# Kernel tuning notes

Hardware: AMD Instinct MI355X
Metric: run time of the kernel (lower is better)

Reference implementation:

```python
import jax, jax.numpy as jnp
import numpy as np

E, K, MULT = 8, 2, 4          # num_experts, top_k, ffn mult
CF = 1.25                     # capacity_factor


def setup_inputs() -> dict:
    key = jax.random.key(0)
    ks = jax.random.split(key, 8)
    B, T, C = 4, 2048, 1024
    H = C * MULT
    s = 0.02
    return {
        "x": jax.random.normal(ks[0], (B, T, C), jnp.float32),
        "rw": jax.random.normal(ks[1], (E, C), jnp.float32) * s,   # router weight [E,C]
        "rb": jnp.zeros((E,), jnp.float32),                        # router bias
        "w1": jax.random.normal(ks[2], (E, C, H), jnp.float32) * s,
        "b1": jnp.zeros((E, H), jnp.float32),
        "w2": jax.random.normal(ks[3], (E, H, C), jnp.float32) * s,
        "b2": jnp.zeros((E, C), jnp.float32),
    }


def reference(x, rw, rb, w1, b1, w2, b2):
    B, T, C = x.shape
    N = B * T
    cap = int(CF * N / E)                      # static capacity per expert
    xf = x.reshape(N, C)
    logits = xf @ rw.T + rb                    # [N,E]
    probs = jax.nn.softmax(logits, axis=-1)
    topk_probs, topk_idx = jax.lax.top_k(probs, K)      # [N,K]
    topk_probs = topk_probs / topk_probs.sum(-1, keepdims=True)

    # Flatten (token, choice) row-major == torch.where(mask) ordering
    flat_idx = topk_idx.reshape(-1)            # [N*K] expert id per slot
    flat_gate = topk_probs.reshape(-1)         # [N*K]
    onehot = jax.nn.one_hot(flat_idx, E, dtype=jnp.int32)          # [N*K,E]
    pos = (jnp.cumsum(onehot, axis=0) - 1)[jnp.arange(N * K), flat_idx]  # rank within expert
    keep = pos < cap                           # first-come-first-served capacity drop
    tok = jnp.arange(N * K) // K               # owning token of each slot

    # Dispatch into [E, cap] buffers; dropped slots go to a dump slot at the end
    buf = jnp.where(keep, flat_idx * cap + pos, E * cap)
    gate_buf = jnp.zeros(E * cap + 1, x.dtype).at[buf].add(flat_gate)[:E * cap]
    tok_buf = jnp.zeros(E * cap + 1, jnp.int32).at[buf].set(tok)[:E * cap]

    inp = xf[tok_buf].reshape(E, cap, C)       # gathered expert inputs
    h = jax.nn.gelu(jnp.einsum('eic,ech->eih', inp, w1) + b1[:, None, :], approximate=False)
    out = jnp.einsum('eih,ehc->eic', h, w2) + b2[:, None, :]
    out = out * gate_buf.reshape(E, cap, 1)    # empty slots have gate 0 -> zero contribution

    y = jnp.zeros((N, C), x.dtype).at[tok_buf].add(out.reshape(E * cap, C))

    # Aux load-balancing loss
    imp = probs.sum(0)
    imp = imp / imp.sum()
    load = jnp.minimum(onehot.sum(0).astype(x.dtype), cap)   # kept token counts
    load = load / load.sum()
    aux_loss = (imp * load).sum() * (E ** 2)
    return y.reshape(B, T, C), aux_loss
```

## Files before the change

kernel.cpp:

```cpp
#include <hip/hip_runtime.h>
#include <hip/hip_bf16.h>
#include <math.h>

#define NE    8
#define KTOP  2
#define CDIM  1024
#define HDIM  4096
#define NTOK  8192
#define CAPE  1280
#define NSLOT (NTOK * KTOP)

typedef __bf16 bf16x8 __attribute__((ext_vector_type(8)));
typedef __bf16 bf16x4 __attribute__((ext_vector_type(4)));
typedef float  f32x4  __attribute__((ext_vector_type(4)));

__global__ __launch_bounds__(256) void k_transpose_bf16(
    const float* __restrict__ src, __bf16* __restrict__ dst, int R, int Cc)
{
    __shared__ float tile[32][33];
    const int e  = blockIdx.z;
    const int cb = blockIdx.x * 32;
    const int rb = blockIdx.y * 32;
    const int tx = threadIdx.x, ty = threadIdx.y;
    const float* s = src + (size_t)e * R * Cc;
    __bf16*      d = dst + (size_t)e * R * Cc;
#pragma unroll
    for (int i = 0; i < 32; i += 8)
        tile[ty + i][tx] = s[(size_t)(rb + ty + i) * Cc + cb + tx];
    __syncthreads();
#pragma unroll
    for (int i = 0; i < 32; i += 8)
        d[(size_t)(cb + ty + i) * R + rb + tx] = (__bf16)tile[tx][ty + i];
}

__global__ __launch_bounds__(256) void k_router(
    const float* __restrict__ x, const float* __restrict__ rw,
    const float* __restrict__ rb, float* __restrict__ probs,
    float* __restrict__ gates, int* __restrict__ tidx)
{
    __shared__ float rws[NE * CDIM];
    const int tid = threadIdx.x;
    for (int i = tid; i < NE * CDIM / 4; i += 256)
        ((float4*)rws)[i] = ((const float4*)rw)[i];
    __syncthreads();

    const int wave = tid >> 6, lane = tid & 63;
    const int n = blockIdx.x * 4 + wave;
    const float* xr = x + (size_t)n * CDIM;

    float acc[NE];
#pragma unroll
    for (int e = 0; e < NE; ++e) acc[e] = 0.f;
    for (int j = 0; j < CDIM / 64; ++j) {
        const float xv = xr[j * 64 + lane];
#pragma unroll
        for (int e = 0; e < NE; ++e) acc[e] += xv * rws[e * CDIM + j * 64 + lane];
    }
#pragma unroll
    for (int off = 32; off > 0; off >>= 1) {
#pragma unroll
        for (int e = 0; e < NE; ++e) acc[e] += __shfl_down(acc[e], off);
    }
    if (lane == 0) {
        float mx = -1e30f;
#pragma unroll
        for (int e = 0; e < NE; ++e) { acc[e] += rb[e]; mx = fmaxf(mx, acc[e]); }
        float p[NE], s = 0.f;
#pragma unroll
        for (int e = 0; e < NE; ++e) { p[e] = expf(acc[e] - mx); s += p[e]; }
        const float inv = 1.f / s;
#pragma unroll
        for (int e = 0; e < NE; ++e) { p[e] *= inv; probs[(size_t)n * NE + e] = p[e]; }
        int   i1 = 0;  float v1 = p[0];
        int   i2 = -1; float v2 = -1.f;
#pragma unroll
        for (int e = 1; e < NE; ++e) {
            if (p[e] > v1)      { v2 = v1; i2 = i1; v1 = p[e]; i1 = e; }
            else if (p[e] > v2) { v2 = p[e]; i2 = e; }
        }
        const float gs = 1.f / (v1 + v2);
        gates[n * 2 + 0] = v1 * gs;  gates[n * 2 + 1] = v2 * gs;
        tidx[n * 2 + 0]  = i1;       tidx[n * 2 + 1]  = i2;
    }
}

__global__ __launch_bounds__(256) void k_scan(
    const int* __restrict__ tidx, const float* __restrict__ probs,
    int* __restrict__ slot, int* __restrict__ tok, float* __restrict__ d_aux)
{
    __shared__ int   lcnt[256][NE];
    __shared__ float ps[256][NE];
    const int t = threadIdx.x;

    for (int i = t; i < NE * CAPE; i += 256) tok[i] = 0;

    int c8[NE];
#pragma unroll
    for (int e = 0; e < NE; ++e) c8[e] = 0;
    const int per  = NSLOT / 256;
    const int base = t * per;
    for (int s = 0; s < per; ++s) c8[tidx[base + s]]++;
#pragma unroll
    for (int e = 0; e < NE; ++e) lcnt[t][e] = c8[e];

    float f8[NE];
#pragma unroll
    for (int e = 0; e < NE; ++e) f8[e] = 0.f;
    for (int n = t; n < NTOK; n += 256) {
        const float4 a = *(const float4*)(probs + (size_t)n * NE);
        const float4 b = *(const float4*)(probs + (size_t)n * NE + 4);
        f8[0] += a.x; f8[1] += a.y; f8[2] += a.z; f8[3] += a.w;
        f8[4] += b.x; f8[5] += b.y; f8[6] += b.z; f8[7] += b.w;
    }
#pragma unroll
    for (int e = 0; e < NE; ++e) ps[t][e] = f8[e];

    __syncthreads();

    int pre[NE], tot[NE];
#pragma unroll
    for (int e = 0; e < NE; ++e) { pre[e] = 0; tot[e] = 0; }
    for (int tt = 0; tt < 256; ++tt) {
#pragma unroll
        for (int e = 0; e < NE; ++e) {
            const int v = lcnt[tt][e];
            tot[e] += v;
            if (tt < t) pre[e] += v;
        }
    }
    for (int s = 0; s < per; ++s) {
        const int sg = base + s;
        const int e  = tidx[sg];
        const int p  = pre[e]++;
        if (p < CAPE) { slot[sg] = e * CAPE + p; tok[e * CAPE + p] = sg >> 1; }
        else          { slot[sg] = -1; }
    }
    if (t == 0) {
        float imp[NE], isum = 0.f, ld[NE], lsum = 0.f;
#pragma unroll
        for (int e = 0; e < NE; ++e) {
            float v = 0.f;
            for (int tt = 0; tt < 256; ++tt) v += ps[tt][e];
            imp[e] = v; isum += v;
        }
#pragma unroll
        for (int e = 0; e < NE; ++e) { ld[e] = fminf((float)tot[e], (float)CAPE); lsum += ld[e]; }
        float aux = 0.f;
#pragma unroll
        for (int e = 0; e < NE; ++e) aux += (imp[e] / isum) * (ld[e] / lsum);
        *d_aux = aux * (float)(NE * NE);
    }
}

__global__ __launch_bounds__(256) void k_gather(
    const float* __restrict__ x, const int* __restrict__ tok,
    __bf16* __restrict__ inp)
{
    const int row = blockIdx.x;
    const int t   = threadIdx.x;
    const int tk  = tok[row];
    const float4 v = ((const float4*)(x + (size_t)tk * CDIM))[t];
    bf16x4 o;
    o[0] = (__bf16)v.x; o[1] = (__bf16)v.y; o[2] = (__bf16)v.z; o[3] = (__bf16)v.w;
    *(bf16x4*)(inp + (size_t)row * CDIM + t * 4) = o;
}

#define MFMA_BF16 __builtin_amdgcn_mfma_f32_16x16x32_bf16

template <bool GELU>
__global__ __launch_bounds__(512, 2) void k_gemm8(
    const __bf16* __restrict__ Aall, const __bf16* __restrict__ Ball,
    const float* __restrict__ biasAll, __bf16* __restrict__ Call,
    int Ktot, int Ntot, int NBN, int mtPerE)
{
    __shared__ char lds[131072];

    const int NK  = Ktot >> 6;
    const int nwg = gridDim.x;
    const int cpx = nwg >> 3;
    const int id  = blockIdx.x;
    const int sid = (id & 7) * cpx + (id >> 3);
    const int bm  = sid / NBN, bn = sid % NBN;
    const int e   = bm / mtPerE;

    const size_t row0 = (size_t)bm * 256;
    const int    col0 = bn * 256;

    const __bf16* gA = Aall + row0 * (size_t)Ktot;
    const __bf16* gB = Ball + ((size_t)e * Ntot + col0) * (size_t)Ktot;

    const int tid = threadIdx.x;
    const int w   = tid >> 6, l = tid & 63;
    const int wr  = w >> 2, wc = w & 3;
    const int lr  = l & 15, hi = l >> 4;

    const int srow = (w << 3) + (l >> 3);
    const int kf   = ((l & 7) ^ (l >> 3)) << 3;
    const int swz = (l & 7) << 4;
    const int kb0 = (hi << 4) ^ swz;
    const int kb1 = (64 + (hi << 4)) ^ swz;

    auto STAGE = [&](int buf, int op, int half, int kt) {
        const __bf16* g = (op ? gB : gA)
            + (size_t)(half * 128 + srow) * Ktot + kt * 64 + kf;
        char* d = lds + ((((buf << 1) + op) << 1) + half) * 16384 + w * 1024;
        __builtin_amdgcn_global_load_lds(
            (const __attribute__((address_space(1))) void*)g,
            (__attribute__((address_space(3))) void*)d, 16, 0, 0);
        __builtin_amdgcn_global_load_lds(
            (const __attribute__((address_space(1))) void*)(g + (size_t)64 * Ktot),
            (__attribute__((address_space(3))) void*)(d + 8192), 16, 0, 0);
    };

    STAGE(0, 0, 0, 0); STAGE(0, 0, 1, 0);
    STAGE(0, 1, 0, 0); STAGE(0, 1, 1, 0);
    if (NK > 1) {
        STAGE(1, 1, 0, 1); STAGE(1, 1, 1, 1);
        asm volatile("s_waitcnt vmcnt(4)" ::: "memory");
    } else {
        asm volatile("s_waitcnt vmcnt(0)" ::: "memory");
    }
    __builtin_amdgcn_s_barrier();
    __builtin_amdgcn_sched_barrier(0);

    f32x4 acc[8][4] = {};
    bf16x8 bfr[4][2], a[2][2];

#define PHASE_MFMA(MB)                                                        \
    __builtin_amdgcn_s_barrier();                                             \
    asm volatile("s_waitcnt lgkmcnt(0)" ::: "memory");                        \
    __builtin_amdgcn_sched_barrier(0);                                        \
    __builtin_amdgcn_s_setprio(1);                                            \
    _Pragma("unroll")                                                         \
    for (int mm = 0; mm < 2; ++mm) {                                          \
        _Pragma("unroll")                                                     \
        for (int n = 0; n < 4; ++n) {                                         \
            acc[(MB) + mm][n] = MFMA_BF16(bfr[n][0], a[mm][0], acc[(MB) + mm][n], 0, 0, 0); \
            acc[(MB) + mm][n] = MFMA_BF16(bfr[n][1], a[mm][1], acc[(MB) + mm][n], 0, 0, 0); \
        }                                                                     \
    }                                                                         \
    __builtin_amdgcn_s_setprio(0);                                            \
    __builtin_amdgcn_s_barrier();                                             \
    __builtin_amdgcn_sched_barrier(0);

#define LOAD_A(MB)                                                            \
    _Pragma("unroll")                                                         \
    for (int mm = 0; mm < 2; ++mm) {                                          \
        a[mm][0] = *(const bf16x8*)(Ab + ((MB) + mm) * 2048 + kb0);           \
        a[mm][1] = *(const bf16x8*)(Ab + ((MB) + mm) * 2048 + kb1);           \
    }

#pragma unroll 2
    for (int T = 0; T < NK; ++T) {
        const int cur = T & 1, nxt = cur ^ 1;
        const char* Ab = lds + (((cur << 1) + 0) * 2 + wr) * 16384 + lr * 128;
        const char* Bb = lds + (((cur << 1) + 1) * 2 + (wc >> 1)) * 16384
                             + (wc & 1) * 8192 + lr * 128;

#pragma unroll
        for (int n = 0; n < 4; ++n) {
            bfr[n][0] = *(const bf16x8*)(Bb + n * 2048 + kb0);
            bfr[n][1] = *(const bf16x8*)(Bb + n * 2048 + kb1);
        }
        LOAD_A(0)
        if (T + 1 < NK) STAGE(nxt, 0, 0, T + 1);
        PHASE_MFMA(0)

        LOAD_A(2)
        if (T + 1 < NK) STAGE(nxt, 0, 1, T + 1);
        PHASE_MFMA(2)

        LOAD_A(4)
        if (T + 2 < NK) STAGE(cur, 1, 0, T + 2);
        PHASE_MFMA(4)

        LOAD_A(6)
        if (T + 2 < NK) {
            STAGE(cur, 1, 1, T + 2);
            asm volatile("s_waitcnt vmcnt(4)" ::: "memory");
        } else if (T + 1 < NK) {
            asm volatile("s_waitcnt vmcnt(0)" ::: "memory");
        }
        PHASE_MFMA(6)
    }

    const size_t crow0 = row0 + (size_t)wr * 128;
    const int    ccol0 = col0 + wc * 64;
#pragma unroll
    for (int n = 0; n < 4; ++n) {
        float bb[4] = {0.f, 0.f, 0.f, 0.f};
        if (GELU) {
            const float4 b4 = *(const float4*)(biasAll + (size_t)e * Ntot
                                               + ccol0 + n * 16 + hi * 4);
            bb[0] = b4.x; bb[1] = b4.y; bb[2] = b4.z; bb[3] = b4.w;
        }
#pragma unroll
        for (int m = 0; m < 8; ++m) {
            const f32x4 v = acc[m][n];
            bf16x4 o;
#pragma unroll
            for (int i = 0; i < 4; ++i) {
                float t = v[i];
                if (GELU) {
                    t += bb[i];
                    const float u  = 0.7978845608028654f * (t + 0.044715f * t * t * t);
                    const float ex = __expf(2.f * u);
                    t = t * (1.f - 1.f / (ex + 1.f));
                }
                o[i] = (__bf16)t;
            }
            *(bf16x4*)(Call + (crow0 + m * 16 + lr) * (size_t)Ntot
                       + ccol0 + n * 16 + hi * 4) = o;
        }
    }
}

__global__ __launch_bounds__(256) void k_combine(
    const __bf16* __restrict__ outb, const int* __restrict__ slot,
    const float* __restrict__ gates, const int* __restrict__ tidx,
    const float* __restrict__ b2, float* __restrict__ y)
{
    const int n = blockIdx.x;
    const int t = threadIdx.x;
    const int c = t * 4;
    float r0 = 0.f, r1 = 0.f, r2 = 0.f, r3 = 0.f;
#pragma unroll
    for (int k = 0; k < KTOP; ++k) {
        const int s = slot[n * 2 + k];
        if (s < 0) continue;
        const float g = gates[n * 2 + k];
        const int   e = tidx[n * 2 + k];
        const bf16x4 v = *(const bf16x4*)(outb + (size_t)s * CDIM + c);
        const float4 bb = *(const float4*)(b2 + (size_t)e * CDIM + c);
        r0 += g * ((float)v[0] + bb.x);
        r1 += g * ((float)v[1] + bb.y);
        r2 += g * ((float)v[2] + bb.z);
        r3 += g * ((float)v[3] + bb.w);
    }
    float4 o = make_float4(r0, r1, r2, r3);
    *(float4*)(y + (size_t)n * CDIM + c) = o;
}

extern "C" void kernel_launch(void* const* d_in, const int* in_sizes, int n_in,
                              void* d_out, int out_size, void* d_ws, size_t ws_size,
                              hipStream_t stream)
{
    const float* x  = (const float*)d_in[0];
    const float* rw = (const float*)d_in[1];
    const float* rb = (const float*)d_in[2];
    const float* w1 = (const float*)d_in[3];
    const float* b1 = (const float*)d_in[4];
    const float* w2 = (const float*)d_in[5];
    const float* b2 = (const float*)d_in[6];
    float* y = (float*)d_out;

    char* ws = (char*)d_ws;
    size_t off = 0;
    auto alloc = [&](size_t bytes) -> void* {
        void* p = ws + off;
        off = (off + bytes + 255) & ~(size_t)255;
        return p;
    };
    __bf16* w1t  = (__bf16*)alloc((size_t)NE * CDIM * HDIM * 2);
    __bf16* w2t  = (__bf16*)alloc((size_t)NE * CDIM * HDIM * 2);
    __bf16* inp  = (__bf16*)alloc((size_t)NE * CAPE * CDIM * 2);
    __bf16* hbuf = (__bf16*)alloc((size_t)NE * CAPE * HDIM * 2);
    __bf16* outb = (__bf16*)alloc((size_t)NE * CAPE * CDIM * 2);
    float*  probs = (float*)alloc((size_t)NTOK * NE * 4);
    float*  gates = (float*)alloc((size_t)NTOK * 2 * 4);
    int*    tidx  = (int*)alloc((size_t)NTOK * 2 * 4);
    int*    slot  = (int*)alloc((size_t)NTOK * 2 * 4);
    int*    tok   = (int*)alloc((size_t)NE * CAPE * 4);

    k_transpose_bf16<<<dim3(HDIM / 32, CDIM / 32, NE), dim3(32, 8), 0, stream>>>(
        w1, w1t, CDIM, HDIM);
    k_transpose_bf16<<<dim3(CDIM / 32, HDIM / 32, NE), dim3(32, 8), 0, stream>>>(
        w2, w2t, HDIM, CDIM);

    k_router<<<NTOK / 4, 256, 0, stream>>>(x, rw, rb, probs, gates, tidx);

    k_scan<<<1, 256, 0, stream>>>(tidx, probs, slot, tok, y + (size_t)NTOK * CDIM);

    k_gather<<<NE * CAPE, 256, 0, stream>>>(x, tok, inp);

    k_gemm8<true><<<dim3((HDIM / 256) * (NE * CAPE / 256)), 512, 0, stream>>>(
        inp, w1t, b1, hbuf, CDIM, HDIM, HDIM / 256, CAPE / 256);
    k_gemm8<false><<<dim3((CDIM / 256) * (NE * CAPE / 256)), 512, 0, stream>>>(
        hbuf, w2t, nullptr, outb, HDIM, CDIM, CDIM / 256, CAPE / 256);

    k_combine<<<NTOK, 256, 0, stream>>>(outb, slot, gates, tidx, b2, y);
}
```

Before: 428.4 us.

## Restructure GEMM main loop with full-tile double buffering and inline-asm LDS reads

The GEMM K-loop now stages the whole next A and B tile into the alternate LDS buffer at once and reads fragments with inline ds_read_b128 at immediate offsets. Two A-fragment register sets ping-pong so LDS reads overlap MFMAs, gated by partial lgkmcnt waits, which replaces the per-phase barrier pairs with a single barrier per K step. The weight transpose also now writes packed bf16 pairs from a 1D block. The aim is fewer barriers and address computations and better overlap, but each K step now waits for all global loads (vmcnt(0)), which can expose more memory latency.

```diff
diff --git a/kernel.cpp b/kernel.cpp
--- a/kernel.cpp
+++ b/kernel.cpp
@@ -12,7 +12,11 @@
 
 typedef __bf16 bf16x8 __attribute__((ext_vector_type(8)));
 typedef __bf16 bf16x4 __attribute__((ext_vector_type(4)));
+typedef __bf16 bf16x2 __attribute__((ext_vector_type(2)));
 typedef float  f32x4  __attribute__((ext_vector_type(4)));
+
+#define GAS __attribute__((address_space(1)))
+#define LAS __attribute__((address_space(3)))
 
 __global__ __launch_bounds__(256) void k_transpose_bf16(
     const float* __restrict__ src, __bf16* __restrict__ dst, int R, int Cc)
@@ -21,16 +25,24 @@
     const int e  = blockIdx.z;
     const int cb = blockIdx.x * 32;
     const int rb = blockIdx.y * 32;
-    const int tx = threadIdx.x, ty = threadIdx.y;
+    const int t  = threadIdx.x;
+    const int tx = t & 31, ty = t >> 5;
     const float* s = src + (size_t)e * R * Cc;
     __bf16*      d = dst + (size_t)e * R * Cc;
 #pragma unroll
     for (int i = 0; i < 32; i += 8)
         tile[ty + i][tx] = s[(size_t)(rb + ty + i) * Cc + cb + tx];
     __syncthreads();
-#pragma unroll
-    for (int i = 0; i < 32; i += 8)
-        d[(size_t)(cb + ty + i) * R + rb + tx] = (__bf16)tile[tx][ty + i];
+    const int op  = t & 15;
+    const int oc0 = t >> 4;
+#pragma unroll
+    for (int j = 0; j < 2; ++j) {
+        const int oc = oc0 + j * 16;
+        bf16x2 v;
+        v[0] = (__bf16)tile[op * 2][oc];
+        v[1] = (__bf16)tile[op * 2 + 1][oc];
+        *(bf16x2*)(d + (size_t)(cb + oc) * R + rb + op * 2) = v;
+    }
 }
 
 __global__ __launch_bounds__(256) void k_router(
@@ -166,6 +178,24 @@
 }
 
 #define MFMA_BF16 __builtin_amdgcn_mfma_f32_16x16x32_bf16
+#define DSR(dst, addr, IMM) \
+    asm volatile("ds_read_b128 %0, %1 offset:" #IMM : "=v"(dst) : "v"(addr))
+#define WLG(N)  asm volatile("s_waitcnt lgkmcnt(" #N ")" ::: "memory")
+#define WVM0()  asm volatile("s_waitcnt vmcnt(0)" ::: "memory")
+#define SB0()   __builtin_amdgcn_sched_barrier(0)
+
+#define MFMA_PHASE(MB, AR)                                                    \
+    __builtin_amdgcn_s_setprio(1);                                            \
+    _Pragma("unroll")                                                         \
+    for (int mm = 0; mm < 2; ++mm) {                                          \
+        _Pragma("unroll")                                                     \
+        for (int n = 0; n < 4; ++n) {                                         \
+            acc[(MB) + mm][n] = MFMA_BF16(bfr[n][0], AR[mm][0], acc[(MB) + mm][n], 0, 0, 0); \
+            acc[(MB) + mm][n] = MFMA_BF16(bfr[n][1], AR[mm][1], acc[(MB) + mm][n], 0, 0, 0); \
+        }                                                                     \
+    }                                                                         \
+    __builtin_amdgcn_s_setprio(0);                                            \
+    SB0();
 
 template <bool GELU>
 __global__ __launch_bounds__(512, 2) void k_gemm8(
@@ -176,8 +206,7 @@
     __shared__ char lds[131072];
 
     const int NK  = Ktot >> 6;
-    const int nwg = gridDim.x;
-    const int cpx = nwg >> 3;
+    const int cpx = gridDim.x >> 3;
     const int id  = blockIdx.x;
     const int sid = (id & 7) * cpx + (id >> 3);
     const int bm  = sid / NBN, bn = sid % NBN;
@@ -186,9 +215,6 @@
     const size_t row0 = (size_t)bm * 256;
     const int    col0 = bn * 256;
 
-    const __bf16* gA = Aall + row0 * (size_t)Ktot;
-    const __bf16* gB = Ball + ((size_t)e * Ntot + col0) * (size_t)Ktot;
-
     const int tid = threadIdx.x;
     const int w   = tid >> 6, l = tid & 63;
     const int wr  = w >> 2, wc = w & 3;
@@ -196,92 +222,77 @@
 
     const int srow = (w << 3) + (l >> 3);
     const int kf   = ((l & 7) ^ (l >> 3)) << 3;
-    const int swz = (l & 7) << 4;
-    const int kb0 = (hi << 4) ^ swz;
-    const int kb1 = (64 + (hi << 4)) ^ swz;
-
-    auto STAGE = [&](int buf, int op, int half, int kt) {
-        const __bf16* g = (op ? gB : gA)
-            + (size_t)(half * 128 + srow) * Ktot + kt * 64 + kf;
-        char* d = lds + ((((buf << 1) + op) << 1) + half) * 16384 + w * 1024;
-        __builtin_amdgcn_global_load_lds(
-            (const __attribute__((address_space(1))) void*)g,
-            (__attribute__((address_space(3))) void*)d, 16, 0, 0);
-        __builtin_amdgcn_global_load_lds(
-            (const __attribute__((address_space(1))) void*)(g + (size_t)64 * Ktot),
-            (__attribute__((address_space(3))) void*)(d + 8192), 16, 0, 0);
+    const __bf16* pA = Aall + (row0 + srow) * (size_t)Ktot + kf;
+    const __bf16* pB = Ball + ((size_t)e * Ntot + col0 + srow) * (size_t)Ktot + kf;
+    const size_t rstep = (size_t)64 * Ktot;
+    const unsigned L0  = (unsigned)(size_t)(LAS char*)lds;
+    const unsigned dA0 = L0 + w * 1024;
+    const unsigned dB0 = L0 + 32768 + w * 1024;
+
+    auto STAGE_ALL = [&](unsigned bufbit, int kt) {
+        const __bf16* ga = pA + (size_t)kt * 64;
+        const __bf16* gb = pB + (size_t)kt * 64;
+#pragma unroll
+        for (int h = 0; h < 4; ++h)
+            __builtin_amdgcn_global_load_lds(
+                (const GAS void*)(ga + h * rstep),
+                (LAS void*)(size_t)(dA0 + bufbit + h * 8192), 16, 0, 0);
+#pragma unroll
+        for (int h = 0; h < 4; ++h)
+            __builtin_amdgcn_global_load_lds(
+                (const GAS void*)(gb + h * rstep),
+                (LAS void*)(size_t)(dB0 + bufbit + h * 8192), 16, 0, 0);
     };
 
-    STAGE(0, 0, 0, 0); STAGE(0, 0, 1, 0);
-    STAGE(0, 1, 0, 0); STAGE(0, 1, 1, 0);
-    if (NK > 1) {
-        STAGE(1, 1, 0, 1); STAGE(1, 1, 1, 1);
-        asm volatile("s_waitcnt vmcnt(4)" ::: "memory");
-    } else {
-        asm volatile("s_waitcnt vmcnt(0)" ::: "memory");
-    }
+    const unsigned swz = (l & 7) << 4;
+    const unsigned kb0 = ((unsigned)(hi << 4)) ^ swz;
+    const unsigned kb1 = ((unsigned)(64 + (hi << 4))) ^ swz;
+    const unsigned Abase = L0 + wr * 16384 + lr * 128;
+    const unsigned Bbase = L0 + 32768 + (wc >> 1) * 16384 + (wc & 1) * 8192 + lr * 128;
+
+    STAGE_ALL(0, 0);
+    WVM0();
     __builtin_amdgcn_s_barrier();
-    __builtin_amdgcn_sched_barrier(0);
+    SB0();
 
     f32x4 acc[8][4] = {};
-    bf16x8 bfr[4][2], a[2][2];
-
-#define PHASE_MFMA(MB)                                                        \
-    __builtin_amdgcn_s_barrier();                                             \
-    asm volatile("s_waitcnt lgkmcnt(0)" ::: "memory");                        \
-    __builtin_amdgcn_sched_barrier(0);                                        \
-    __builtin_amdgcn_s_setprio(1);                                            \
-    _Pragma("unroll")                                                         \
-    for (int mm = 0; mm < 2; ++mm) {                                          \
-        _Pragma("unroll")                                                     \
-        for (int n = 0; n < 4; ++n) {                                         \
-            acc[(MB) + mm][n] = MFMA_BF16(bfr[n][0], a[mm][0], acc[(MB) + mm][n], 0, 0, 0); \
-            acc[(MB) + mm][n] = MFMA_BF16(bfr[n][1], a[mm][1], acc[(MB) + mm][n], 0, 0, 0); \
-        }                                                                     \
-    }                                                                         \
-    __builtin_amdgcn_s_setprio(0);                                            \
-    __builtin_amdgcn_s_barrier();                                             \
-    __builtin_amdgcn_sched_barrier(0);
-
-#define LOAD_A(MB)                                                            \
-    _Pragma("unroll")                                                         \
-    for (int mm = 0; mm < 2; ++mm) {                                          \
-        a[mm][0] = *(const bf16x8*)(Ab + ((MB) + mm) * 2048 + kb0);           \
-        a[mm][1] = *(const bf16x8*)(Ab + ((MB) + mm) * 2048 + kb1);           \
-    }
-
-#pragma unroll 2
+    bf16x8 bfr[4][2], aX[2][2], aY[2][2];
+
+    unsigned cb = 0;
     for (int T = 0; T < NK; ++T) {
-        const int cur = T & 1, nxt = cur ^ 1;
-        const char* Ab = lds + (((cur << 1) + 0) * 2 + wr) * 16384 + lr * 128;
-        const char* Bb = lds + (((cur << 1) + 1) * 2 + (wc >> 1)) * 16384
-                             + (wc & 1) * 8192 + lr * 128;
-
-#pragma unroll
-        for (int n = 0; n < 4; ++n) {
-            bfr[n][0] = *(const bf16x8*)(Bb + n * 2048 + kb0);
-            bfr[n][1] = *(const bf16x8*)(Bb + n * 2048 + kb1);
-        }
-        LOAD_A(0)
-        if (T + 1 < NK) STAGE(nxt, 0, 0, T + 1);
-        PHASE_MFMA(0)
-
-        LOAD_A(2)
-        if (T + 1 < NK) STAGE(nxt, 0, 1, T + 1);
-        PHASE_MFMA(2)
-
-        LOAD_A(4)
-        if (T + 2 < NK) STAGE(cur, 1, 0, T + 2);
-        PHASE_MFMA(4)
-
-        LOAD_A(6)
-        if (T + 2 < NK) {
-            STAGE(cur, 1, 1, T + 2);
-            asm volatile("s_waitcnt vmcnt(4)" ::: "memory");
-        } else if (T + 1 < NK) {
-            asm volatile("s_waitcnt vmcnt(0)" ::: "memory");
-        }
-        PHASE_MFMA(6)
+        const unsigned nb = cb ^ 65536u;
+        const unsigned va0 = Abase + cb + kb0, va1 = Abase + cb + kb1;
+        const unsigned vb0 = Bbase + cb + kb0, vb1 = Bbase + cb + kb1;
+
+        DSR(bfr[0][0], vb0, 0);    DSR(bfr[0][1], vb1, 0);
+        DSR(bfr[1][0], vb0, 2048); DSR(bfr[1][1], vb1, 2048);
+        DSR(bfr[2][0], vb0, 4096); DSR(bfr[2][1], vb1, 4096);
+        DSR(bfr[3][0], vb0, 6144); DSR(bfr[3][1], vb1, 6144);
+        DSR(aX[0][0], va0, 0);     DSR(aX[0][1], va1, 0);
+        DSR(aX[1][0], va0, 2048);  DSR(aX[1][1], va1, 2048);
+
+        if (T + 1 < NK) STAGE_ALL(nb, T + 1);
+
+        DSR(aY[0][0], va0, 4096);  DSR(aY[0][1], va1, 4096);
+        DSR(aY[1][0], va0, 6144);  DSR(aY[1][1], va1, 6144);
+
+        WLG(4); SB0();
+        MFMA_PHASE(0, aX)
+        DSR(aX[0][0], va0, 8192);  DSR(aX[0][1], va1, 8192);
+        DSR(aX[1][0], va0, 10240); DSR(aX[1][1], va1, 10240);
+        WLG(4); SB0();
+        MFMA_PHASE(2, aY)
+        DSR(aY[0][0], va0, 12288); DSR(aY[0][1], va1, 12288);
+        DSR(aY[1][0], va0, 14336); DSR(aY[1][1], va1, 14336);
+        WLG(4); SB0();
+        MFMA_PHASE(4, aX)
+        WLG(0); SB0();
+        MFMA_PHASE(6, aY)
+
+        WVM0();
+        __builtin_amdgcn_s_barrier();
+        SB0();
+        cb = nb;
     }
 
     const size_t crow0 = row0 + (size_t)wr * 128;
@@ -372,9 +383,9 @@
     int*    slot  = (int*)alloc((size_t)NTOK * 2 * 4);
     int*    tok   = (int*)alloc((size_t)NE * CAPE * 4);
 
-    k_transpose_bf16<<<dim3(HDIM / 32, CDIM / 32, NE), dim3(32, 8), 0, stream>>>(
+    k_transpose_bf16<<<dim3(HDIM / 32, CDIM / 32, NE), 256, 0, stream>>>(
         w1, w1t, CDIM, HDIM);
-    k_transpose_bf16<<<dim3(CDIM / 32, HDIM / 32, NE), dim3(32, 8), 0, stream>>>(
+    k_transpose_bf16<<<dim3(CDIM / 32, HDIM / 32, NE), 256, 0, stream>>>(
         w2, w2t, HDIM, CDIM);
 
     k_router<<<NTOK / 4, 256, 0, stream>>>(x, rw, rb, probs, gates, tidx);
```

Measured after the change: 427.6 us. About the same (-0.2%).
